# Kernel tuning notes

Measured on AMD Instinct MI355X. Metric: run time of the kernel, lower is better.

## Reference

```python
import jax, jax.numpy as jnp
import numpy as np

N = 32768   # 'a' nodes
K = 8       # incoming edges per node (regular graph)
K2 = K // 2
E = N * K   # edges, stored as reverse pairs (2i, 2i+1)
D = 300     # hid_dim
H = 4       # attention heads
DEPTH = 3


def _build_graph():
    i = np.arange(N)
    src = np.empty(E, np.int64)
    mail = np.empty((N, K), np.int64)
    for d in range(1, K2 + 1):
        base = 2 * (i * K2 + (d - 1))
        src[base] = i                 # edge i -> (i+d)%N
        src[base + 1] = (i + d) % N   # reverse edge (i+d)%N -> i
        # incoming edges of node v: ((v-d)->v) and ((v+d)->v)
        mail[:, 2 * (d - 1)] = 2 * (((i - d) % N) * K2 + (d - 1))
        mail[:, 2 * (d - 1) + 1] = 2 * (i * K2 + (d - 1)) + 1
    return src, mail


def setup_inputs() -> dict:
    key = jax.random.key(0)
    ks = jax.random.split(key, 12)
    s = 1.0 / np.sqrt(D)
    src, mail = _build_graph()
    return {
        'f': jax.random.normal(ks[0], (N, D), jnp.float32),
        'x': jax.random.normal(ks[1], (E, D), jnp.float32),
        'mail_idx': jnp.asarray(mail),
        'src_idx': jnp.asarray(src),
        'Wq': jax.random.normal(ks[2], (D, D), jnp.float32) * s,
        'bq': jnp.zeros((D,), jnp.float32),
        'Wk': jax.random.normal(ks[3], (D, D), jnp.float32) * s,
        'bk': jnp.zeros((D,), jnp.float32),
        'Wv': jax.random.normal(ks[4], (D, D), jnp.float32) * s,
        'bv': jnp.zeros((D,), jnp.float32),
        'Wo': jax.random.normal(ks[5], (D, D), jnp.float32) * s,
        'bo': jnp.zeros((D,), jnp.float32),
        'Wmp': jax.random.normal(ks[6], (DEPTH - 1, D, D), jnp.float32) * s,
        'bmp': jnp.zeros((DEPTH - 1, D), jnp.float32),
        'Wlast': jax.random.normal(ks[7], (3 * D, D), jnp.float32) * s,
        'blast': jnp.zeros((D,), jnp.float32),
    }


def _mha(q_in, k_in, v_in, Wq, bq, Wk, bk, Wv, bv, Wo, bo):
    # q_in: [N,1,D], k_in/v_in: [N,K,D]  (per-node neighborhood attention)
    dk = D // H
    q = (q_in @ Wq + bq).reshape(N, 1, H, dk).transpose(0, 2, 1, 3)
    k = (k_in @ Wk + bk).reshape(N, -1, H, dk).transpose(0, 2, 1, 3)
    v = (v_in @ Wv + bv).reshape(N, -1, H, dk).transpose(0, 2, 1, 3)
    scores = jnp.einsum('nhqd,nhkd->nhqk', q, k) / jnp.sqrt(jnp.float32(dk))
    p = jax.nn.softmax(scores, axis=-1)
    o = jnp.einsum('nhqk,nhkd->nhqd', p, v).transpose(0, 2, 1, 3).reshape(N, 1, D)
    return o @ Wo + bo


def reference(f, x, mail_idx, src_idx, Wq, bq, Wk, bk, Wv, bv, Wo, bo,
              Wmp, bmp, Wlast, blast):
    rev = jnp.arange(E) ^ 1  # reverse_edge: swap within consecutive pairs
    f_h = f              # init_node: f_h = f.clone()
    h = x                # init_edge: h = x.clone()
    for i in range(DEPTH - 1):
        mail = h[mail_idx]                    # copy_e mailbox [N,K,D]
        feat = f_h[:, None, :]                # [N,1,D]
        # add_attn: attn(feat, mail, mail + feat)
        f_h = _mha(feat, mail, mail + feat,
                   Wq, bq, Wk, bk, Wv, bv, Wo, bo)[:, 0, :]
        rev_h = h[rev]                        # paired reverse-edge feature
        m = f_h[src_idx] - rev_h              # del_reverse_message
        h = jax.nn.relu(x + m @ Wmp[i] + bmp[i])  # update_edge
    # final node update: Linear(cat([sum(mailbox h), f_h, f]))
    mail_sum = jnp.sum(h[mail_idx], axis=1)   # [N,D]
    f_final = jnp.concatenate([mail_sum, f_h, f], axis=1) @ Wlast + blast
    return f_final
```

## Files before the change

### kernel.cpp

```cpp
#include <hip/hip_runtime.h>

typedef unsigned short u16;
typedef unsigned int u32;
typedef __bf16 bf16x8 __attribute__((ext_vector_type(8)));
typedef float f32x4 __attribute__((ext_vector_type(4)));

#define N_NODES 32768
#define E_EDGES 262144
#define BQ_U16 26240
#define S75 0.11547005383792515f

__device__ __forceinline__ float b2f(u16 u) {
    union { u32 u; float f; } x; x.u = ((u32)u) << 16; return x.f;
}
__device__ __forceinline__ u16 f2b(float f) {
    union { float f; u32 u; } x; x.f = f;
    u32 r = x.u + 0x7FFF + ((x.u >> 16) & 1);
    return (u16)(r >> 16);
}

#define GLOAD16(g, l) \
    __builtin_amdgcn_global_load_lds((const __attribute__((address_space(1))) u32*)(g), \
                                     (__attribute__((address_space(3))) u32*)(l), 16, 0, 0)

__global__ void convT_k(const float* __restrict__ src, int R, int C,
                        u16* __restrict__ dst, int KP_, long total) {
    long id = (long)blockIdx.x * blockDim.x + threadIdx.x;
    if (id >= total) return;
    int n = (int)(id / KP_), k = (int)(id % KP_);
    dst[id] = (k < R && n < C) ? f2b(src[(long)k * C + n]) : (u16)0;
}

__global__ void convTq_k(const float* __restrict__ src, u16* __restrict__ dst) {
    int id = blockIdx.x * 256 + threadIdx.x;
    if (id >= 4 * BQ_U16) return;
    int q = id / BQ_U16, rem = id % BQ_U16;
    int r = rem / 328, c = rem % 328;
    int n = q * 80 + r;
    dst[id] = (c < 300 && n < 300) ? f2b(src[(long)c * 300 + n]) : (u16)0;
}

__global__ void wqkq_k(const float* __restrict__ Wq, const float* __restrict__ Wk,
                       u16* __restrict__ dst) {
    int id = blockIdx.x * 256 + threadIdx.x;
    if (id >= 16 * BQ_U16) return;
    int q = id / BQ_U16, rem = id % BQ_U16;
    int r = rem / 328, c = rem % 328;
    int h = q >> 2;
    int cc = (q & 3) * 80 + r;
    float acc = 0.f;
    if (c < 300 && cc < 300) {
        const float* wq = Wq + (long)c * 300 + 75 * h;
        const float* wk = Wk + (long)cc * 300 + 75 * h;
        for (int d = 0; d < 75; ++d) acc += wq[d] * wk[d];
        acc *= S75;
    }
    dst[id] = f2b(acc);
}

__global__ void bqk_k(const float* __restrict__ bq, const float* __restrict__ Wk,
                      float* __restrict__ dst) {
    int n = blockIdx.x * 256 + threadIdx.x;
    if (n >= 1280) return;
    int h = n / 320, cc = n % 320;
    float acc = 0.f;
    if (cc < 300) {
        const float* b = bq + 75 * h;
        const float* wk = Wk + (long)cc * 300 + 75 * h;
        for (int d = 0; d < 75; ++d) acc += b[d] * wk[d];
        acc *= S75;
    }
    dst[n] = acc;
}

__global__ void ucatp_k(const float* __restrict__ Wv, const float* __restrict__ Wo,
                        u16* __restrict__ dst) {
    long id = (long)blockIdx.x * 256 + threadIdx.x;
    if (id >= 4L * 5 * BQ_U16) return;
    int q = (int)(id / (5 * BQ_U16));
    int rem = (int)(id % (5 * BQ_U16));
    int ph = rem / BQ_U16;
    int rem2 = rem % BQ_U16;
    int r = rem2 / 328, c = rem2 % 328;
    int n = q * 80 + r;
    float acc = 0.f;
    if (n < 300 && c < 320) {
        if (ph < 4) {
            int a = c;
            if (a < 300) {
                const float* wv = Wv + (long)a * 300 + 75 * ph;
                const float* wo = Wo + (long)(75 * ph) * 300 + n;
                for (int d = 0; d < 75; ++d) acc += wv[d] * wo[(long)d * 300];
            }
        } else {
            int a = c;
            if (a < 300) {
                const float* wv = Wv + (long)a * 300;
                const float* wo = Wo + n;
                for (int d = 0; d < 300; ++d) acc += wv[d] * wo[(long)d * 300];
            }
        }
    }
    dst[id] = f2b(acc);
}

__global__ void bvo_k(const float* __restrict__ bv, const float* __restrict__ Wo,
                      const float* __restrict__ bo, float* __restrict__ dst) {
    int n = blockIdx.x * 256 + threadIdx.x;
    if (n >= 320) return;
    float acc = 0.f;
    if (n < 300) {
        for (int d = 0; d < 300; ++d) acc += bv[d] * Wo[(long)d * 300 + n];
        acc += bo[n];
    }
    dst[n] = acc;
}

__global__ void padb_k(const float* __restrict__ bmp, float* __restrict__ dst) {
    int id = blockIdx.x * 256 + threadIdx.x;
    if (id >= 640) return;
    int it = id / 320, c = id % 320;
    dst[id] = (c < 300) ? bmp[it * 300 + c] : 0.f;
}

__global__ void padconv_k(const float* __restrict__ src, int C,
                          u16* __restrict__ dst, int CP,
                          u16* __restrict__ dst2, int CP2, long total) {
    long id = (long)blockIdx.x * blockDim.x + threadIdx.x;
    if (id >= total) return;
    int cw = CP >> 3;
    long row = id / cw;
    int c8 = (int)(id % cw) * 8;
    u32 w[4];
    #pragma unroll
    for (int p = 0; p < 4; ++p) {
        int c0 = c8 + 2 * p, c1 = c0 + 1;
        u16 lo = (c0 < C) ? f2b(src[row * C + c0]) : (u16)0;
        u16 hi = (c1 < C) ? f2b(src[row * C + c1]) : (u16)0;
        w[p] = (u32)lo | ((u32)hi << 16);
    }
    u32* d = (u32*)(dst + row * CP + c8);
    d[0] = w[0]; d[1] = w[1]; d[2] = w[2]; d[3] = w[3];
    if (dst2) {
        u32* d2 = (u32*)(dst2 + row * CP2 + c8);
        d2[0] = w[0]; d2[1] = w[1]; d2[2] = w[2]; d2[3] = w[3];
    }
}

__global__ void featcopy_k(const u16* __restrict__ src, u16* __restrict__ dst) {
    long id = (long)blockIdx.x * 256 + threadIdx.x;
    if (id >= (long)N_NODES * 40) return;
    long row = id / 40;
    int c8 = (int)(id % 40) * 8;
    *(uint4*)&dst[row * 1600 + 1280 + c8] = *(const uint4*)&src[row * 320 + c8];
}


#define PG_SHARED \
    __shared__ __attribute__((aligned(16))) u16 Al[128 * 328]; \
    __shared__ __attribute__((aligned(16))) u16 Bs[80 * 328];

#define PG_PRE \
    const int tid = threadIdx.x; \
    const int w = tid >> 6, lane = tid & 63; \
    const int tl = lane & 15, thi = lane >> 4; \
    const long m0 = (long)blockIdx.x * 128; \
    const int w_u = __builtin_amdgcn_readfirstlane(w); \
     \
    _Pragma("unroll") \
    for (int j = 0; j < 10; ++j) { \
        int slot = j * 512 + tid; \
        int r = slot / 41, s = slot % 41; \
        GLOAD16(A + (m0 + r) * 320L + (s < 40 ? s : 39) * 8, \
                &Al[(j * 512 + w_u * 64) * 8]); \
    } \
    if (tid < 128) { \
        int slot = 5120 + tid; \
        int r = slot / 41, s = slot % 41; \
        GLOAD16(A + (m0 + r) * 320L + (s < 40 ? s : 39) * 8, \
                &Al[(5120 + w_u * 64) * 8]); \
    }

#define PG_STAGEB(QQ) { \
    const u16* Bsrc_ = Bq + (QQ) * BQ_U16; \
    _Pragma("unroll") \
    for (int j = 0; j < 7; ++j) { \
        int t = j * 512 + tid; \
        if (t < 3280) \
            GLOAD16(Bsrc_ + (long)t * 8, &Bs[(j * 512 + w_u * 64) * 8]); \
    } }

#define PG_COMPUTE \
    f32x4 acc[5]; \
    _Pragma("unroll") for (int fc = 0; fc < 5; ++fc) acc[fc] = (f32x4)(0.f); \
    _Pragma("unroll") \
    for (int KB = 0; KB < 10; ++KB) { \
        bf16x8 a_ = *(const bf16x8*)&Al[(w * 16 + tl) * 328 + thi * 8 + KB * 32]; \
        __builtin_amdgcn_s_setprio(1); \
        _Pragma("unroll") for (int fc = 0; fc < 5; ++fc) { \
            bf16x8 bb_ = *(const bf16x8*)&Bs[(fc * 16 + tl) * 328 + thi * 8 + KB * 32]; \
            acc[fc] = __builtin_amdgcn_mfma_f32_16x16x32_bf16(bb_, a_, acc[fc], 0, 0, 0); \
        } \
        __builtin_amdgcn_s_setprio(0); \
    }

template<int NPH, int OSTR>
__global__ __launch_bounds__(512, 2) void pgemm_k(
    const u16* __restrict__ A, const u16* __restrict__ Bq,
    const float* __restrict__ bias, u16* __restrict__ outB)
{
    PG_SHARED
    PG_PRE
    PG_STAGEB(0)
    const long row = m0 + w * 16 + tl;

    for (int q = 0; q < NPH; ++q) {
        __syncthreads();
        PG_COMPUTE
        __syncthreads();
        if (q + 1 < NPH) PG_STAGEB(q + 1)
        #pragma unroll
        for (int fc = 0; fc < 5; ++fc) {
            const int c0 = q * 80 + fc * 16 + thi * 4;
            f32x4 v = acc[fc];
            if (bias) {
                const float4 bs = *(const float4*)&bias[c0];
                v[0] += bs.x; v[1] += bs.y; v[2] += bs.z; v[3] += bs.w;
            }
            uint2 p;
            p.x = (u32)f2b(v[0]) | ((u32)f2b(v[1]) << 16);
            p.y = (u32)f2b(v[2]) | ((u32)f2b(v[3]) << 16);
            *(uint2*)&outB[row * (long)OSTR + c0] = p;
        }
    }
}

__global__ __launch_bounds__(512, 2) void phgemm_k(
    const u16* __restrict__ A , const u16* __restrict__ Bq ,
    const u16* __restrict__ FG, const u16* __restrict__ hx,
    const int* __restrict__ srcidx, const float* __restrict__ bias ,
    u16* __restrict__ outB)
{
    PG_SHARED
    PG_PRE
    PG_STAGEB(0)
    const long row = m0 + w * 16 + tl;
    const int srow = srcidx[row];

    for (int q = 0; q < 4; ++q) {
        __syncthreads();
        PG_COMPUTE
        __syncthreads();
        if (q + 1 < 4) PG_STAGEB(q + 1)
        #pragma unroll
        for (int fc = 0; fc < 5; ++fc) {
            const int c0 = q * 80 + fc * 16 + thi * 4;
            float o0 = __shfl_xor(acc[fc][0], 1, 64);
            float o1 = __shfl_xor(acc[fc][1], 1, 64);
            float o2 = __shfl_xor(acc[fc][2], 1, 64);
            float o3 = __shfl_xor(acc[fc][3], 1, 64);
            const ushort4 fg = *(const ushort4*)&FG[(long)srow * 320 + c0];
            const ushort4 xv = *(const ushort4*)&hx[row * 320 + c0];
            const float4 bs = *(const float4*)&bias[c0];
            float v0 = b2f(fg.x) + b2f(xv.x) - o0 + bs.x;
            float v1 = b2f(fg.y) + b2f(xv.y) - o1 + bs.y;
            float v2 = b2f(fg.z) + b2f(xv.z) - o2 + bs.z;
            float v3 = b2f(fg.w) + b2f(xv.w) - o3 + bs.w;
            v0 = fmaxf(v0, 0.f); v1 = fmaxf(v1, 0.f);
            v2 = fmaxf(v2, 0.f); v3 = fmaxf(v3, 0.f);
            uint2 p;
            p.x = (u32)f2b(v0) | ((u32)f2b(v1) << 16);
            p.y = (u32)f2b(v2) | ((u32)f2b(v3) << 16);
            *(uint2*)&outB[row * 320 + c0] = p;
        }
    }
}

#define TCOMP(KB, APTR) do { \
    bf16x8 av_[2], bb_[5]; \
    _Pragma("unroll") for (int fr = 0; fr < 2; ++fr) \
        av_[fr] = *(const bf16x8*)&(APTR)[ar0 + fr * 512]; \
    _Pragma("unroll") for (int fc = 0; fc < 5; ++fc) \
        bb_[fc] = *(const bf16x8*)&Bsw[br0 + fc * 5248 + (KB) * 32]; \
    __builtin_amdgcn_s_setprio(1); \
    _Pragma("unroll") for (int fr = 0; fr < 2; ++fr) \
        _Pragma("unroll") for (int fc = 0; fc < 5; ++fc) \
            acc[fr][fc] = __builtin_amdgcn_mfma_f32_16x16x32_bf16(bb_[fc], av_[fr], acc[fr][fc], 0, 0, 0); \
    __builtin_amdgcn_s_setprio(0); \
} while (0)

__global__ __launch_bounds__(256, 2) void wgemm_k(
    const u16* __restrict__ A , const u16* __restrict__ Bp,
    const float* __restrict__ bias, u16* __restrict__ outB)
{
    __shared__ __attribute__((aligned(16))) u16 Bsw[80 * 328];
    __shared__ __attribute__((aligned(16))) u16 As3[3][128 * 32];
    const int tid = threadIdx.x;
    const int wf = tid >> 6, lane = tid & 63;
    const int tl = lane & 15, thi = lane >> 4;
    const int bid = blockIdx.x;
    const int gid = (bid & 7) * ((int)gridDim.x >> 3) + (bid >> 3);
    const long m0 = (long)(gid >> 2) * 128;
    const int q = gid & 3;
    const int n0 = q * 80;
    const int wf_u = __builtin_amdgcn_readfirstlane(wf);
    const u16* BsrcQ = Bp + (long)q * (5 * BQ_U16);

    const int r1 = tid >> 2;
    const int g1 = (tid & 3) ^ ((r1 >> 1) & 3);
    const u16* gA0 = A + (m0 + r1) * 1600L + g1 * 8;
    const u16* gA1 = A + (m0 + 64 + r1) * 1600L + g1 * 8;

    f32x4 acc[2][5];
    #pragma unroll
    for (int i = 0; i < 2; ++i)
        #pragma unroll
        for (int j = 0; j < 5; ++j) acc[i][j] = (f32x4)(0.f);
    const int ar0 = (wf * 32 + tl) * 32 + (thi ^ ((tl >> 1) & 3)) * 8;
    const int br0 = tl * 328 + thi * 8;

    #pragma unroll
    for (int ph = 0; ph < 5; ++ph) {
        if (ph) __syncthreads();
        const u16* Bsrc = BsrcQ + ph * BQ_U16;
        #pragma unroll
        for (int i = 0; i < 13; ++i) {
            int t = i * 256 + tid;
            if (t < 3280)
                GLOAD16(Bsrc + (long)t * 8, &Bsw[(i * 256 + wf_u * 64) * 8]);
        }
        const long ko = (long)ph * 320;

#define WSTAGE(KB) { \
    GLOAD16(gA0 + ko + (KB) * 32, &As3[(KB) % 3][wf_u * 512]); \
    GLOAD16(gA1 + ko + (KB) * 32, &As3[(KB) % 3][2048 + wf_u * 512]); }

        WSTAGE(0); WSTAGE(1);

#define WSTEP(KB, VN) { \
    asm volatile("s_waitcnt vmcnt(" #VN ")" ::: "memory"); \
    __builtin_amdgcn_s_barrier(); \
    __builtin_amdgcn_sched_barrier(0); \
    if ((KB) + 2 < 10) WSTAGE((KB) + 2); \
    TCOMP(KB, (&As3[(KB) % 3][0])); }

        WSTEP(0, 2) WSTEP(1, 2) WSTEP(2, 2) WSTEP(3, 2) WSTEP(4, 2)
        WSTEP(5, 2) WSTEP(6, 2) WSTEP(7, 2) WSTEP(8, 2) WSTEP(9, 0)
#undef WSTEP
#undef WSTAGE
    }

    #pragma unroll
    for (int fr = 0; fr < 2; ++fr) {
        const long row = m0 + wf * 32 + fr * 16 + tl;
        #pragma unroll
        for (int fc = 0; fc < 5; ++fc) {
            const int c0 = n0 + fc * 16 + thi * 4;
            f32x4 v = acc[fr][fc];
            const float4 bs = *(const float4*)&bias[c0];
            v[0] += bs.x; v[1] += bs.y; v[2] += bs.z; v[3] += bs.w;
            uint2 p;
            p.x = (u32)f2b(v[0]) | ((u32)f2b(v[1]) << 16);
            p.y = (u32)f2b(v[2]) | ((u32)f2b(v[3]) << 16);
            *(uint2*)&outB[row * 320 + c0] = p;
        }
    }
}

__global__ __launch_bounds__(256) void attn2_k(
    const u16* __restrict__ qg, const u16* __restrict__ hcur,
    const int* __restrict__ mail, u16* __restrict__ wideA)
{
    const int tid = threadIdx.x;
    const long n = (long)blockIdx.x * 4 + (tid >> 6);
    const int lane = tid & 63;
    const bool act = lane < 40;
    const int ll = act ? lane : 39;

    int idx[8];
    #pragma unroll
    for (int j = 0; j < 8; ++j) idx[j] = mail[n * 8 + j];
    uint4 hr[8];
    #pragma unroll
    for (int j = 0; j < 8; ++j)
        hr[j] = *(const uint4*)&hcur[(long)idx[j] * 320 + ll * 8];
    uint4 qv[4];
    #pragma unroll
    for (int h = 0; h < 4; ++h)
        qv[h] = *(const uint4*)&qg[n * 1280 + h * 320 + ll * 8];
    if (!act) {
        #pragma unroll
        for (int j = 0; j < 8; ++j) hr[j] = make_uint4(0, 0, 0, 0);
    }

    float qf[4][8];
    #pragma unroll
    for (int h = 0; h < 4; ++h) {
        const u32 w[4] = {qv[h].x, qv[h].y, qv[h].z, qv[h].w};
        #pragma unroll
        for (int p = 0; p < 4; ++p) {
            qf[h][2 * p]     = b2f((u16)(w[p] & 0xFFFF));
            qf[h][2 * p + 1] = b2f((u16)(w[p] >> 16));
        }
    }

    float s[4][8];
    #pragma unroll
    for (int j = 0; j < 8; ++j) {
        float hf[8];
        const u32 w[4] = {hr[j].x, hr[j].y, hr[j].z, hr[j].w};
        #pragma unroll
        for (int p = 0; p < 4; ++p) {
            hf[2 * p]     = b2f((u16)(w[p] & 0xFFFF));
            hf[2 * p + 1] = b2f((u16)(w[p] >> 16));
        }
        #pragma unroll
        for (int h = 0; h < 4; ++h) {
            float d = 0.f;
            #pragma unroll
            for (int m = 0; m < 8; ++m) d += qf[h][m] * hf[m];
            d += __shfl_xor(d, 32, 64);
            d += __shfl_xor(d, 16, 64);
            d += __shfl_xor(d, 8, 64);
            d += __shfl_xor(d, 4, 64);
            d += __shfl_xor(d, 2, 64);
            d += __shfl_xor(d, 1, 64);
            s[h][j] = d;
        }
    }

    float p_[4][8];
    #pragma unroll
    for (int h = 0; h < 4; ++h) {
        float mx = s[h][0];
        #pragma unroll
        for (int j = 1; j < 8; ++j) mx = fmaxf(mx, s[h][j]);
        float sum = 0.f;
        #pragma unroll
        for (int j = 0; j < 8; ++j) { p_[h][j] = __expf(s[h][j] - mx); sum += p_[h][j]; }
        const float inv = 1.f / sum;
        #pragma unroll
        for (int j = 0; j < 8; ++j) p_[h][j] *= inv;
    }

    float y[4][8];
    #pragma unroll
    for (int h = 0; h < 4; ++h)
        #pragma unroll
        for (int m = 0; m < 8; ++m) y[h][m] = 0.f;
    #pragma unroll
    for (int j = 0; j < 8; ++j) {
        float hf[8];
        const u32 w[4] = {hr[j].x, hr[j].y, hr[j].z, hr[j].w};
        #pragma unroll
        for (int p = 0; p < 4; ++p) {
            hf[2 * p]     = b2f((u16)(w[p] & 0xFFFF));
            hf[2 * p + 1] = b2f((u16)(w[p] >> 16));
        }
        #pragma unroll
        for (int h = 0; h < 4; ++h)
            #pragma unroll
            for (int m = 0; m < 8; ++m) y[h][m] += p_[h][j] * hf[m];
    }
    if (act) {
        #pragma unroll
        for (int h = 0; h < 4; ++h) {
            uint4 o;
            o.x = (u32)f2b(y[h][0]) | ((u32)f2b(y[h][1]) << 16);
            o.y = (u32)f2b(y[h][2]) | ((u32)f2b(y[h][3]) << 16);
            o.z = (u32)f2b(y[h][4]) | ((u32)f2b(y[h][5]) << 16);
            o.w = (u32)f2b(y[h][6]) | ((u32)f2b(y[h][7]) << 16);
            *(uint4*)&wideA[n * 1600 + h * 320 + lane * 8] = o;
        }
    }
}

#define LOADB(bq, kt1) { const long ko_ = (long)(kt1) << 6; \
    _Pragma("unroll") for (int fc = 0; fc < 5; ++fc) \
      _Pragma("unroll") for (int ks = 0; ks < 2; ++ks) \
        bq[fc][ks] = *(const bf16x8*)(gBw + (long)fc * 16 * KP + ko_ + ks * 32); }

#define READA(lkt) { \
    _Pragma("unroll") for (int fr = 0; fr < 4; ++fr) \
      _Pragma("unroll") for (int ks = 0; ks < 2; ++ks) \
        a[fr][ks] = *(const bf16x8*)&As[(fr * 16 + tl) * 320 + ((((lkt) * 8 + ks * 4 + thi) ^ sx) * 8)]; }

#define DOMFMA(bq) { _Pragma("unroll") for (int fr = 0; fr < 4; ++fr) \
    _Pragma("unroll") for (int fc = 0; fc < 5; ++fc) \
      _Pragma("unroll") for (int ks = 0; ks < 2; ++ks) \
        acc[fr][fc] = __builtin_amdgcn_mfma_f32_16x16x32_bf16(bq[fc][ks], a[fr][ks], acc[fr][fc], 0, 0, 0); }

template<int KP>
__global__ __launch_bounds__(256, 2) void gemm_k(
    const u16* __restrict__ A,
    const u16* __restrict__ BT,
    const float* __restrict__ bias,
    float* __restrict__ outF, int ostride, int ocols)
{
    __shared__ u16 As[64 * 320];
    const int tid = threadIdx.x;
    const int w = tid >> 6, lane = tid & 63;
    const int tl = lane & 15, thi = lane >> 4;
    const int sx = tl & 7;
    const long m0 = (long)blockIdx.x * 64;
    const int w_u = __builtin_amdgcn_readfirstlane(w);

    const u16* gBw = BT + ((long)(w * 80 + tl)) * KP + thi * 8;

    f32x4 acc[4][5];
    #pragma unroll
    for (int i = 0; i < 4; ++i)
        #pragma unroll
        for (int j = 0; j < 5; ++j) acc[i][j] = (f32x4)(0.f);

    constexpr int NCH = KP / 320;
    constexpr int NST = KP >> 6;
    bf16x8 bA[5][2], bB[5][2], a[4][2];

    #pragma unroll
    for (int kb = 0; kb < NCH; ++kb) {
        if (kb) __syncthreads();
        #pragma unroll
        for (int i = 0; i < 10; ++i) {
            const int c = i * 256 + w_u * 64 + lane;
            const int r = c / 40, s = c - r * 40;
            GLOAD16(A + (m0 + r) * (long)KP + kb * 320 + ((s ^ (r & 7)) * 8),
                    &As[(i * 256 + w_u * 64) * 8]);
        }
        if (kb == 0) LOADB(bA, 0);
        __syncthreads();
        #pragma unroll
        for (int lkt = 0; lkt < 5; ++lkt) {
            const int kt = kb * 5 + lkt;
            if (kt + 1 < NST) {
                if (kt & 1) { LOADB(bA, kt + 1); } else { LOADB(bB, kt + 1); }
            }
            READA(lkt);
            if (kt & 1) { DOMFMA(bB); } else { DOMFMA(bA); }
        }
    }

    #pragma unroll
    for (int fr = 0; fr < 4; ++fr) {
        const long row = m0 + fr * 16 + tl;
        #pragma unroll
        for (int fc = 0; fc < 5; ++fc) {
            const int c0 = w * 80 + fc * 16 + thi * 4;
            f32x4 v = acc[fr][fc];
            if (bias && c0 < 300) {
                const float4 bs = *(const float4*)&bias[c0];
                v[0] += bs.x; v[1] += bs.y; v[2] += bs.z; v[3] += bs.w;
            }
            if (c0 < ocols)
                *(float4*)&outF[row * (long)ostride + c0] = make_float4(v[0], v[1], v[2], v[3]);
        }
    }
}

__global__ __launch_bounds__(256) void concat_k(
    const u16* __restrict__ hb, const u16* __restrict__ fhb,
    const float* __restrict__ f, const int* __restrict__ mail,
    u16* __restrict__ Acat)
{
    const long n = blockIdx.x;
    int m[8];
    #pragma unroll
    for (int j = 0; j < 8; ++j) m[j] = mail[n * 8 + j];
    for (int c = threadIdx.x; c < 960; c += 256) {
        float v;
        if (c < 300) {
            float s = 0.f;
            #pragma unroll
            for (int j = 0; j < 8; ++j) s += b2f(hb[(long)m[j] * 320 + c]);
            v = s;
        } else if (c < 600) v = b2f(fhb[n * 320 + (c - 300)]);
        else if (c < 900) v = f[n * 300 + (c - 600)];
        else v = 0.f;
        Acat[n * 960 + c] = f2b(v);
    }
}

extern "C" void kernel_launch(void* const* d_in, const int* in_sizes, int n_in,
                              void* d_out, int out_size, void* d_ws, size_t ws_size,
                              hipStream_t stream)
{
    const int N = N_NODES, E = E_EDGES;
    const float* f    = (const float*)d_in[0];
    const float* x    = (const float*)d_in[1];
    const int*   mail = (const int*)d_in[2];
    const int*   srcx = (const int*)d_in[3];
    const float* Wq = (const float*)d_in[4];   const float* bq = (const float*)d_in[5];
    const float* Wk = (const float*)d_in[6];
    const float* Wv = (const float*)d_in[8];   const float* bv = (const float*)d_in[9];
    const float* Wo = (const float*)d_in[10];  const float* bo = (const float*)d_in[11];
    const float* Wmp = (const float*)d_in[12]; const float* bmp = (const float*)d_in[13];
    const float* Wlast = (const float*)d_in[14]; const float* blast = (const float*)d_in[15];
    float* out = (float*)d_out;

    char* ws = (char*)d_ws;
    size_t off = 0;
    auto alloc = [&](size_t b) -> void* {
        void* p = ws + off; off += (b + 255) & ~(size_t)255; return p;
    };
    u16* hb    = (u16*)alloc((size_t)E * 320 * 2);
    u16* hb2   = (u16*)alloc((size_t)E * 320 * 2);
    u16* qgb   = (u16*)alloc((size_t)N * 1280 * 2);
    u16* wideA = (u16*)alloc((size_t)N * 1600 * 2);
    u16* fhb   = (u16*)alloc((size_t)N * 320 * 2);
    u16* FGb   = (u16*)alloc((size_t)N * 320 * 2);
    u16* Acat  = (u16*)alloc((size_t)N * 960 * 2);
    u16* WqkS  = (u16*)alloc((size_t)16 * BQ_U16 * 2);
    u16* Wm0S  = (u16*)alloc((size_t)4 * BQ_U16 * 2);
    u16* Wm1S  = (u16*)alloc((size_t)4 * BQ_U16 * 2);
    u16* UcatP = (u16*)alloc((size_t)4 * 5 * BQ_U16 * 2);
    u16* WcatB = (u16*)alloc((size_t)960 * 320 * 2);
    float* bqkF = (float*)alloc(1280 * 4);
    float* bvoF = (float*)alloc(320 * 4);
    float* bmpP = (float*)alloc(640 * 4);

    {
        wqkq_k<<<(16 * BQ_U16 + 255) / 256, 256, 0, stream>>>(Wq, Wk, WqkS);
        bqk_k<<<5, 256, 0, stream>>>(bq, Wk, bqkF);
        ucatp_k<<<(int)((4L * 5 * BQ_U16 + 255) / 256), 256, 0, stream>>>(Wv, Wo, UcatP);
        bvo_k<<<2, 256, 0, stream>>>(bv, Wo, bo, bvoF);
        padb_k<<<3, 256, 0, stream>>>(bmp, bmpP);
        int blks = (4 * BQ_U16 + 255) / 256;
        convTq_k<<<blks, 256, 0, stream>>>(Wmp, Wm0S);
        convTq_k<<<blks, 256, 0, stream>>>(Wmp + 90000, Wm1S);
        long totc = (long)320 * 960;
        convT_k<<<(int)((totc + 255) / 256), 256, 0, stream>>>(Wlast, 900, 300, WcatB, 960, totc);
    }
    {
        long totE = (long)E * 40;
        padconv_k<<<(int)((totE + 255) / 256), 256, 0, stream>>>(x, 300, hb, 320, nullptr, 0, totE);
        long totN = (long)N * 40;
        padconv_k<<<(int)((totN + 255) / 256), 256, 0, stream>>>(f, 300, fhb, 320, wideA + 1280, 1600, totN);
    }

    const int GN = N / 128;
    const int GE = E / 128;
    const int GNW = (N / 128) * 4;

    for (int it = 0; it < 2; ++it) {
        const u16* WmS = it ? Wm1S : Wm0S;
        const u16* hcur = it ? hb2 : hb;
        u16* hnxt = it ? hb : hb2;
        pgemm_k<16, 1280><<<GN, 512, 0, stream>>>(fhb, WqkS, bqkF, qgb);
        attn2_k<<<N / 4, 256, 0, stream>>>(qgb, hcur, mail, wideA);
        wgemm_k<<<GNW, 256, 0, stream>>>(wideA, UcatP, bvoF, fhb);
        featcopy_k<<<(int)(((long)N * 40 + 255) / 256), 256, 0, stream>>>(fhb, wideA);
        pgemm_k<4, 320><<<GN, 512, 0, stream>>>(fhb, WmS, nullptr, FGb);
        phgemm_k<<<GE, 512, 0, stream>>>(hcur, WmS, FGb, hb, srcx, bmpP + it * 320, hnxt);
    }

    concat_k<<<N, 256, 0, stream>>>(hb, fhb, f, mail, Acat);
    gemm_k<960><<<N / 64, 256, 0, stream>>>(Acat, WcatB, blast, out, 300, 300);
}
```

Baseline: 1.409 ms.

## Restructure edge GEMM into 256-row tiles with K-split and double-buffered weights

The edge-update GEMM (phgemm_k) now handles 256 edge rows per block instead of 128. It splits the K dimension into two halves of 160 and keeps accumulators for all 320 output columns in registers. Weight slices are prestored in a new half-K padded layout and staged into two alternating LDS buffers, so loading the next slice overlaps the MFMA work on the current one, and the full epilogue runs after both K halves. This is meant to reuse each A tile across all output columns and cut the barrier-separated stage/compute serialisation. The cost is a large register footprint (40 f32x4 accumulators per thread), which may lower occupancy or cause spills.

New measurement: 1.366 ms. 3.1% less time.

```diff
diff --git a/kernel.cpp b/kernel.cpp
--- a/kernel.cpp
+++ b/kernel.cpp
@@ -8,6 +8,8 @@
 #define N_NODES 32768
 #define E_EDGES 262144
 #define BQ_U16 26240
+#define BH184 14720
+#define WMQH_U16 117760
 #define S75 0.11547005383792515f
 
 __device__ __forceinline__ float b2f(u16 u) {
@@ -38,6 +40,18 @@
     int r = rem / 328, c = rem % 328;
     int n = q * 80 + r;
     dst[id] = (c < 300 && n < 300) ? f2b(src[(long)c * 300 + n]) : (u16)0;
+}
+
+__global__ void convTqh_k(const float* __restrict__ src, u16* __restrict__ dst) {
+    long id = (long)blockIdx.x * 256 + threadIdx.x;
+    if (id >= WMQH_U16) return;
+    int qh = (int)(id / BH184), rem = (int)(id % BH184);
+    int q = qh >> 1, kh = qh & 1;
+    int r = rem / 184, kk = rem % 184;
+    int n = q * 80 + r, k = kh * 160 + kk;
+    u16 v = 0;
+    if (n < 300 && kk < 160 && k < 300) v = f2b(src[(long)k * 300 + n]);
+    dst[id] = v;
 }
 
 __global__ void wqkq_k(const float* __restrict__ Wq, const float* __restrict__ Wk,
@@ -155,7 +169,6 @@
     *(uint4*)&dst[row * 1600 + 1280 + c8] = *(const uint4*)&src[row * 320 + c8];
 }
 
-
 #define PG_SHARED \
     __shared__ __attribute__((aligned(16))) u16 Al[128 * 328]; \
     __shared__ __attribute__((aligned(16))) u16 Bs[80 * 328];
@@ -166,7 +179,6 @@
     const int tl = lane & 15, thi = lane >> 4; \
     const long m0 = (long)blockIdx.x * 128; \
     const int w_u = __builtin_amdgcn_readfirstlane(w); \
-     \
     _Pragma("unroll") \
     for (int j = 0; j < 10; ++j) { \
         int slot = j * 512 + tid; \
@@ -236,42 +248,106 @@
 }
 
 __global__ __launch_bounds__(512, 2) void phgemm_k(
-    const u16* __restrict__ A , const u16* __restrict__ Bq ,
+    const u16* __restrict__ A , const u16* __restrict__ Bqh ,
     const u16* __restrict__ FG, const u16* __restrict__ hx,
     const int* __restrict__ srcidx, const float* __restrict__ bias ,
     u16* __restrict__ outB)
 {
-    PG_SHARED
-    PG_PRE
-    PG_STAGEB(0)
-    const long row = m0 + w * 16 + tl;
-    const int srow = srcidx[row];
-
-    for (int q = 0; q < 4; ++q) {
-        __syncthreads();
-        PG_COMPUTE
-        __syncthreads();
-        if (q + 1 < 4) PG_STAGEB(q + 1)
-        #pragma unroll
-        for (int fc = 0; fc < 5; ++fc) {
-            const int c0 = q * 80 + fc * 16 + thi * 4;
-            float o0 = __shfl_xor(acc[fc][0], 1, 64);
-            float o1 = __shfl_xor(acc[fc][1], 1, 64);
-            float o2 = __shfl_xor(acc[fc][2], 1, 64);
-            float o3 = __shfl_xor(acc[fc][3], 1, 64);
-            const ushort4 fg = *(const ushort4*)&FG[(long)srow * 320 + c0];
-            const ushort4 xv = *(const ushort4*)&hx[row * 320 + c0];
-            const float4 bs = *(const float4*)&bias[c0];
-            float v0 = b2f(fg.x) + b2f(xv.x) - o0 + bs.x;
-            float v1 = b2f(fg.y) + b2f(xv.y) - o1 + bs.y;
-            float v2 = b2f(fg.z) + b2f(xv.z) - o2 + bs.z;
-            float v3 = b2f(fg.w) + b2f(xv.w) - o3 + bs.w;
-            v0 = fmaxf(v0, 0.f); v1 = fmaxf(v1, 0.f);
-            v2 = fmaxf(v2, 0.f); v3 = fmaxf(v3, 0.f);
-            uint2 p;
-            p.x = (u32)f2b(v0) | ((u32)f2b(v1) << 16);
-            p.y = (u32)f2b(v2) | ((u32)f2b(v3) << 16);
-            *(uint2*)&outB[row * 320 + c0] = p;
+    __shared__ __attribute__((aligned(16))) u16 Al[256 * 184];
+    __shared__ __attribute__((aligned(16))) u16 Bs2[2][80 * 184];
+    const int tid = threadIdx.x;
+    const int w = tid >> 6, lane = tid & 63;
+    const int tl = lane & 15, thi = lane >> 4;
+    const long m0 = (long)blockIdx.x * 256;
+    const int w_u = __builtin_amdgcn_readfirstlane(w);
+
+#define PH_STAGEA(KH) { \
+    _Pragma("unroll") \
+    for (int i = 0; i < 12; ++i) { \
+        int c = i * 512 + tid; \
+        if (c < 5888) { \
+            int r_ = c / 23, s_ = c % 23; \
+            int ss_ = s_ < 20 ? s_ : 19; \
+            GLOAD16(A + (m0 + r_) * 320L + (KH) * 160 + ss_ * 8, \
+                    &Al[(i * 512 + w_u * 64) * 8]); \
+        } \
+    } }
+
+#define PH_STAGEB(P, BUF) { \
+    const u16* bsrc_ = Bqh + (long)((((P) & 3) * 2 + ((P) >> 2)) * BH184); \
+    _Pragma("unroll") \
+    for (int i = 0; i < 4; ++i) { \
+        int c = i * 512 + tid; \
+        if (c < 1840) \
+            GLOAD16(bsrc_ + (long)c * 8, &Bs2[BUF][(i * 512 + w_u * 64) * 8]); \
+    } }
+
+    f32x4 acc[4][2][5];
+    #pragma unroll
+    for (int q = 0; q < 4; ++q)
+        #pragma unroll
+        for (int i = 0; i < 2; ++i)
+            #pragma unroll
+            for (int j = 0; j < 5; ++j) acc[q][i][j] = (f32x4)(0.f);
+
+#define PH_COMP(Q, BUF) { \
+    _Pragma("unroll") \
+    for (int ks = 0; ks < 5; ++ks) { \
+        bf16x8 a0_ = *(const bf16x8*)&Al[(w * 32 + tl) * 184 + thi * 8 + ks * 32]; \
+        bf16x8 a1_ = *(const bf16x8*)&Al[(w * 32 + 16 + tl) * 184 + thi * 8 + ks * 32]; \
+        __builtin_amdgcn_s_setprio(1); \
+        _Pragma("unroll") for (int fc = 0; fc < 5; ++fc) { \
+            bf16x8 b_ = *(const bf16x8*)&Bs2[BUF][(fc * 16 + tl) * 184 + thi * 8 + ks * 32]; \
+            acc[Q][0][fc] = __builtin_amdgcn_mfma_f32_16x16x32_bf16(b_, a0_, acc[Q][0][fc], 0, 0, 0); \
+            acc[Q][1][fc] = __builtin_amdgcn_mfma_f32_16x16x32_bf16(b_, a1_, acc[Q][1][fc], 0, 0, 0); } \
+        __builtin_amdgcn_s_setprio(0); \
+    } }
+
+    PH_STAGEA(0)
+    PH_STAGEB(0, 0)
+    __syncthreads();
+    PH_STAGEB(1, 1) PH_COMP(0, 0) __syncthreads();
+    PH_STAGEB(2, 0) PH_COMP(1, 1) __syncthreads();
+    PH_STAGEB(3, 1) PH_COMP(2, 0) __syncthreads();
+    PH_COMP(3, 1) __syncthreads();
+    PH_STAGEA(1)
+    PH_STAGEB(4, 0)
+    __syncthreads();
+    PH_STAGEB(5, 1) PH_COMP(0, 0) __syncthreads();
+    PH_STAGEB(6, 0) PH_COMP(1, 1) __syncthreads();
+    PH_STAGEB(7, 1) PH_COMP(2, 0) __syncthreads();
+    PH_COMP(3, 1)
+#undef PH_COMP
+#undef PH_STAGEB
+#undef PH_STAGEA
+
+    #pragma unroll
+    for (int fr = 0; fr < 2; ++fr) {
+        const long row = m0 + w * 32 + fr * 16 + tl;
+        const int srow = srcidx[row];
+        #pragma unroll
+        for (int q = 0; q < 4; ++q) {
+            #pragma unroll
+            for (int fc = 0; fc < 5; ++fc) {
+                const int c0 = q * 80 + fc * 16 + thi * 4;
+                float o0 = __shfl_xor(acc[q][fr][fc][0], 1, 64);
+                float o1 = __shfl_xor(acc[q][fr][fc][1], 1, 64);
+                float o2 = __shfl_xor(acc[q][fr][fc][2], 1, 64);
+                float o3 = __shfl_xor(acc[q][fr][fc][3], 1, 64);
+                const ushort4 fg = *(const ushort4*)&FG[(long)srow * 320 + c0];
+                const ushort4 xv = *(const ushort4*)&hx[row * 320 + c0];
+                const float4 bs = *(const float4*)&bias[c0];
+                float v0 = b2f(fg.x) + b2f(xv.x) - o0 + bs.x;
+                float v1 = b2f(fg.y) + b2f(xv.y) - o1 + bs.y;
+                float v2 = b2f(fg.z) + b2f(xv.z) - o2 + bs.z;
+                float v3 = b2f(fg.w) + b2f(xv.w) - o3 + bs.w;
+                v0 = fmaxf(v0, 0.f); v1 = fmaxf(v1, 0.f);
+                v2 = fmaxf(v2, 0.f); v3 = fmaxf(v3, 0.f);
+                uint2 p;
+                p.x = (u32)f2b(v0) | ((u32)f2b(v1) << 16);
+                p.y = (u32)f2b(v2) | ((u32)f2b(v3) << 16);
+                *(uint2*)&outB[row * 320 + c0] = p;
+            }
         }
     }
 }
@@ -612,6 +688,8 @@
     u16* WqkS  = (u16*)alloc((size_t)16 * BQ_U16 * 2);
     u16* Wm0S  = (u16*)alloc((size_t)4 * BQ_U16 * 2);
     u16* Wm1S  = (u16*)alloc((size_t)4 * BQ_U16 * 2);
+    u16* Wm0H  = (u16*)alloc((size_t)WMQH_U16 * 2);
+    u16* Wm1H  = (u16*)alloc((size_t)WMQH_U16 * 2);
     u16* UcatP = (u16*)alloc((size_t)4 * 5 * BQ_U16 * 2);
     u16* WcatB = (u16*)alloc((size_t)960 * 320 * 2);
     float* bqkF = (float*)alloc(1280 * 4);
@@ -627,6 +705,9 @@
         int blks = (4 * BQ_U16 + 255) / 256;
         convTq_k<<<blks, 256, 0, stream>>>(Wmp, Wm0S);
         convTq_k<<<blks, 256, 0, stream>>>(Wmp + 90000, Wm1S);
+        int blksh = (WMQH_U16 + 255) / 256;
+        convTqh_k<<<blksh, 256, 0, stream>>>(Wmp, Wm0H);
+        convTqh_k<<<blksh, 256, 0, stream>>>(Wmp + 90000, Wm1H);
         long totc = (long)320 * 960;
         convT_k<<<(int)((totc + 255) / 256), 256, 0, stream>>>(Wlast, 900, 300, WcatB, 960, totc);
     }
@@ -638,11 +719,12 @@
     }
 
     const int GN = N / 128;
-    const int GE = E / 128;
+    const int GE2 = E / 256;
     const int GNW = (N / 128) * 4;
 
     for (int it = 0; it < 2; ++it) {
         const u16* WmS = it ? Wm1S : Wm0S;
+        const u16* WmH = it ? Wm1H : Wm0H;
         const u16* hcur = it ? hb2 : hb;
         u16* hnxt = it ? hb : hb2;
         pgemm_k<16, 1280><<<GN, 512, 0, stream>>>(fhb, WqkS, bqkF, qgb);
@@ -650,7 +732,7 @@
         wgemm_k<<<GNW, 256, 0, stream>>>(wideA, UcatP, bvoF, fhb);
         featcopy_k<<<(int)(((long)N * 40 + 255) / 256), 256, 0, stream>>>(fhb, wideA);
         pgemm_k<4, 320><<<GN, 512, 0, stream>>>(fhb, WmS, nullptr, FGb);
-        phgemm_k<<<GE, 512, 0, stream>>>(hcur, WmS, FGb, hb, srcx, bmpP + it * 320, hnxt);
+        phgemm_k<<<GE2, 512, 0, stream>>>(hcur, WmH, FGb, hb, srcx, bmpP + it * 320, hnxt);
     }
 
     concat_k<<<N, 256, 0, stream>>>(hb, fhb, f, mail, Acat);
```
